# Optimization experiments

Measured on AMD Instinct MI355X. Metric: run time of the kernel, lower is better.

The kernel has to match this reference:

```python
import jax, jax.numpy as jnp
import numpy as np

NUM_HEADS = 8
FREQ_RATIO = 0.5


def _resize_bilinear(img, out_h, out_w):
    """Bilinear resize of last two dims, matching torch interpolate align_corners=False."""
    in_h, in_w = img.shape[-2], img.shape[-1]

    def idx(in_size, out_size):
        src = jnp.maximum((jnp.arange(out_size, dtype=jnp.float32) + 0.5) * (in_size / out_size) - 0.5, 0.0)
        i0 = jnp.floor(src).astype(jnp.int32)
        i1 = jnp.minimum(i0 + 1, in_size - 1)
        w = src - i0.astype(jnp.float32)
        return i0, i1, w

    r0, r1, wr = idx(in_h, out_h)
    img = img[..., r0, :] * (1.0 - wr)[:, None] + img[..., r1, :] * wr[:, None]
    c0, c1, wc = idx(in_w, out_w)
    img = img[..., c0] * (1.0 - wc) + img[..., c1] * wc
    return img


def setup_inputs() -> dict:
    key = jax.random.key(0)
    ks = jax.random.split(key, 6)
    B, T, J, C = 4, 256, 17, 512
    H = NUM_HEADS
    x = jax.random.normal(ks[0], (B, T, J, C), dtype=jnp.float32)
    att_map = jax.random.uniform(ks[1], (B, H, J, T, T), dtype=jnp.float32)
    weight = jax.random.uniform(ks[2], (1,), dtype=jnp.float32)
    w_qkv = jax.random.normal(ks[3], (C, 3 * C), dtype=jnp.float32) * 0.02
    w_proj = jax.random.normal(ks[4], (C, C), dtype=jnp.float32) * 0.02
    b_proj = jnp.zeros((C,), dtype=jnp.float32)
    freq_gate = jnp.ones((1,), dtype=jnp.float32)
    return {"x": x, "att_map": att_map, "weight": weight, "w_qkv": w_qkv,
            "w_proj": w_proj, "b_proj": b_proj, "freq_gate": freq_gate}


def reference(x, att_map, weight, w_qkv, w_proj, b_proj, freq_gate):
    B, T, J, C = x.shape
    H = NUM_HEADS
    d = C // H
    scale = d ** (-0.5)

    qkv = (x @ w_qkv).reshape(B, T, J, 3, H, d)
    qkv = jnp.transpose(qkv, (3, 0, 4, 2, 1, 5))  # [3,B,H,J,T,d]
    q, k, v = qkv[0], qkv[1], qkv[2]

    # time-domain attention over T, per (B,H,J)
    attn_time = jax.nn.softmax(jnp.einsum('bhjtd,bhjsd->bhjts', q, k) * scale, axis=-1)

    # frequency-domain attention
    qf = jnp.fft.rfft(q, axis=3)
    kf = jnp.fft.rfft(k, axis=3)
    F = qf.shape[3]                      # T//2 + 1
    keep = max(1, int(F * FREQ_RATIO))
    qf = qf[:, :, :, :keep]
    kf = kf[:, :, :, :keep]
    af = jnp.einsum('bhjfd,bhjgd->bhjfg', qf, jnp.conj(kf)) * scale  # complex [B,H,J,keep,keep]
    # torch combines softmax(real) + 1j*softmax(imag); only the real part survives
    af_real = jax.nn.softmax(af.real, axis=-1)
    af_real = jnp.pad(af_real, ((0, 0), (0, 0), (0, 0), (0, F - keep), (0, 0)))  # zero-pad rows to F
    attn_freq = _resize_bilinear(af_real, T, T)  # [B,H,J,T,T]

    gate = jax.nn.sigmoid(freq_gate)  # broadcastable scalar
    attn_self = gate * attn_freq + (1.0 - gate) * attn_time
    attn = weight * attn_self + (1.0 - weight) * att_map

    out = jnp.einsum('bhjts,bhjsd->bhjtd', attn, v)        # [B,H,J,T,d]
    out = jnp.transpose(out, (0, 3, 2, 1, 4)).reshape(B, T, J, C)
    return out @ w_proj + b_proj
```

## Files before the change

### kernel.cpp

```cpp
#include <hip/hip_runtime.h>
#include <hip/hip_bf16.h>


#define SCALE 0.125f
#define LSTR 72

typedef __attribute__((ext_vector_type(4))) float f32x4;
typedef __attribute__((ext_vector_type(8))) short bf16x8;
typedef __attribute__((ext_vector_type(8))) unsigned short u16x8;

__device__ __forceinline__ float bf2f(unsigned short u) {
  return __uint_as_float(((unsigned int)u) << 16);
}
__device__ __forceinline__ unsigned short f2bf(float f) {
  unsigned int u = __float_as_uint(f);
  u += 0x7FFFu + ((u >> 16) & 1u);
  return (unsigned short)(u >> 16);
}

__global__ __launch_bounds__(256) void conv_x(
    const float* __restrict__ x, unsigned short* __restrict__ xh,
    unsigned short* __restrict__ xl) {
  const size_t i = ((size_t)blockIdx.x * 256 + threadIdx.x) * 8;
  float4 a = *(const float4*)(x + i);
  float4 b = *(const float4*)(x + i + 4);
  float vv[8] = {a.x, a.y, a.z, a.w, b.x, b.y, b.z, b.w};
  u16x8 hi, lo;
#pragma unroll
  for (int e = 0; e < 8; ++e) {
    unsigned short h = f2bf(vv[e]);
    hi[e] = h;
    lo[e] = f2bf(vv[e] - bf2f(h));
  }
  *(u16x8*)&xh[i] = hi;
  *(u16x8*)&xl[i] = lo;
}

__global__ __launch_bounds__(256) void conv_wT(
    const float* __restrict__ w, unsigned short* __restrict__ th,
    unsigned short* __restrict__ tl, int N) {
  __shared__ float T[64][65];
  const int tid = threadIdx.x;
  const int nt = blockIdx.x * 64, kt = blockIdx.y * 64;
  for (int i = tid; i < 4096; i += 256) {
    const int r = i >> 6, c = i & 63;
    T[r][c] = w[(size_t)(kt + r) * N + nt + c];
  }
  __syncthreads();
  for (int i = tid; i < 4096; i += 256) {
    const int rn = i >> 6, ck = i & 63;
    const float v = T[ck][rn];
    const unsigned short h = f2bf(v);
    const size_t o = (size_t)(nt + rn) * 512 + kt + ck;
    th[o] = h;
    tl[o] = f2bf(v - bf2f(h));
  }
}

__global__ __launch_bounds__(256, 2) void qkv_gemm(
    const unsigned short* __restrict__ xh, const unsigned short* __restrict__ xl,
    const unsigned short* __restrict__ wh, const unsigned short* __restrict__ wl,
    unsigned short* __restrict__ qh, unsigned short* __restrict__ ql,
    unsigned short* __restrict__ kh, unsigned short* __restrict__ kl,
    unsigned short* __restrict__ vt) {
  __shared__ __attribute__((aligned(16))) unsigned short Wt[2][128 * LSTR];
  __shared__ __attribute__((aligned(16))) unsigned short Xt[2][128 * LSTR];

  const int tid = threadIdx.x;
  const int bx = blockIdx.x, by = blockIdx.y;
  const int wid = tid >> 6, lane = tid & 63;
  const int lr = lane & 15, lg = lane >> 4;
  const int wr = wid >> 1, wc = wid & 1;
  const int srow = tid >> 3, skg = tid & 7;

  const unsigned short* xhp = xh + (size_t)(by * 128 + srow) * 512 + skg * 8;
  const unsigned short* xlp = xl + (size_t)(by * 128 + srow) * 512 + skg * 8;
  const unsigned short* whp = wh + (size_t)(bx * 128 + srow) * 512 + skg * 8;
  const unsigned short* wlp = wl + (size_t)(bx * 128 + srow) * 512 + skg * 8;

  u16x8 rxh[4], rxl[4], rwh[4], rwl[4];
  auto loadk = [&](int k0) {
#pragma unroll
    for (int it = 0; it < 4; ++it) {
      const size_t o = (size_t)(32 * it) * 512 + k0;
      rxh[it] = *(const u16x8*)(xhp + o);
      rxl[it] = *(const u16x8*)(xlp + o);
      rwh[it] = *(const u16x8*)(whp + o);
      rwl[it] = *(const u16x8*)(wlp + o);
    }
  };

  f32x4 acc[4][4];
#pragma unroll
  for (int nt = 0; nt < 4; ++nt)
#pragma unroll
    for (int mt = 0; mt < 4; ++mt) acc[nt][mt] = (f32x4){0.f, 0.f, 0.f, 0.f};

  loadk(0);
  for (int s = 0; s < 8; ++s) {
    if (s) __syncthreads();
#pragma unroll
    for (int it = 0; it < 4; ++it) {
      const int base = (srow + 32 * it) * LSTR + skg * 8;
      *(u16x8*)&Xt[0][base] = rxh[it];
      *(u16x8*)&Xt[1][base] = rxl[it];
      *(u16x8*)&Wt[0][base] = rwh[it];
      *(u16x8*)&Wt[1][base] = rwl[it];
    }
    __syncthreads();
    if (s < 7) loadk((s + 1) * 64);
#pragma unroll
    for (int kh2 = 0; kh2 < 2; ++kh2) {
      const int kbase = kh2 * 32 + lg * 8;
      bf16x8 Ah[4], Al[4], Bh[4], Bl[4];
#pragma unroll
      for (int nt = 0; nt < 4; ++nt) {
        const int n = wr * 64 + nt * 16 + lr;
        Ah[nt] = *(bf16x8*)&Wt[0][n * LSTR + kbase];
        Al[nt] = *(bf16x8*)&Wt[1][n * LSTR + kbase];
      }
#pragma unroll
      for (int mt = 0; mt < 4; ++mt) {
        const int m = wc * 64 + mt * 16 + lr;
        Bh[mt] = *(bf16x8*)&Xt[0][m * LSTR + kbase];
        Bl[mt] = *(bf16x8*)&Xt[1][m * LSTR + kbase];
      }
#pragma unroll
      for (int nt = 0; nt < 4; ++nt)
#pragma unroll
        for (int mt = 0; mt < 4; ++mt) {
          acc[nt][mt] = __builtin_amdgcn_mfma_f32_16x16x32_bf16(Ah[nt], Bh[mt], acc[nt][mt], 0, 0, 0);
          acc[nt][mt] = __builtin_amdgcn_mfma_f32_16x16x32_bf16(Ah[nt], Bl[mt], acc[nt][mt], 0, 0, 0);
          acc[nt][mt] = __builtin_amdgcn_mfma_f32_16x16x32_bf16(Al[nt], Bh[mt], acc[nt][mt], 0, 0, 0);
        }
    }
  }

#pragma unroll
  for (int mt = 0; mt < 4; ++mt) {
    const int m = by * 128 + wc * 64 + mt * 16 + lr;
    const int jj = m % 17;
    const int bt = m / 17;
    const int t = bt & 255;
    const int b = bt >> 8;
#pragma unroll
    for (int nt = 0; nt < 4; ++nt) {
      const int c = bx * 128 + wr * 64 + nt * 16 + lg * 4;
      const int qi = c >> 9;
      const int h = (c >> 6) & 7;
      const int dd = c & 63;
      const size_t hdbase = ((size_t)((b * 8 + h) * 17 + jj)) * 16384;
      float a0 = acc[nt][mt][0], a1 = acc[nt][mt][1], a2 = acc[nt][mt][2],
            a3 = acc[nt][mt][3];
      ushort4 hi4 = make_ushort4(f2bf(a0), f2bf(a1), f2bf(a2), f2bf(a3));
      if (qi == 2) {
        vt[hdbase + (size_t)(dd + 0) * 256 + t] = hi4.x;
        vt[hdbase + (size_t)(dd + 1) * 256 + t] = hi4.y;
        vt[hdbase + (size_t)(dd + 2) * 256 + t] = hi4.z;
        vt[hdbase + (size_t)(dd + 3) * 256 + t] = hi4.w;
      } else {
        ushort4 lo4 = make_ushort4(f2bf(a0 - bf2f(hi4.x)), f2bf(a1 - bf2f(hi4.y)),
                                   f2bf(a2 - bf2f(hi4.z)), f2bf(a3 - bf2f(hi4.w)));
        unsigned short* dh = qi ? kh : qh;
        unsigned short* dl = qi ? kl : ql;
        *(ushort4*)&dh[hdbase + t * 64 + dd] = hi4;
        *(ushort4*)&dl[hdbase + t * 64 + dd] = lo4;
      }
    }
  }
}

__global__ __launch_bounds__(256) void freq_kernel(
    const unsigned short* __restrict__ qhp, const unsigned short* __restrict__ qlp,
    const unsigned short* __restrict__ khp, const unsigned short* __restrict__ klp,
    unsigned short* __restrict__ af_out) {
  __shared__ __attribute__((aligned(16))) unsigned short qT[2][64 * 256];
  __shared__ __attribute__((aligned(16))) unsigned short QF[4][64 * 64];
  __shared__ __attribute__((aligned(16))) unsigned short KF[4][64 * 64];

  const int tid = threadIdx.x;
  const int head = blockIdx.x;
  const int w = tid >> 6, lane = tid & 63;
  const int lr = lane & 15, lg = lane >> 4;
  const int f0 = w << 4;

  bf16x8 Ech[8], Ecl[8], Esh[8], Esl[8];
  {
    const int f = f0 + lr;
#pragma unroll
    for (int kb = 0; kb < 8; ++kb) {
      bf16x8 ch, cl, sh, sl;
#pragma unroll
      for (int i = 0; i < 8; ++i) {
        int t = kb * 32 + lg * 8 + i;
        int idx = (f * t) & 255;
        float s, c;
        __sincosf((float)idx * 0.02454369260617026f, &s, &c);
        unsigned short chh = f2bf(c);
        unsigned short shh = f2bf(s);
        ch[i] = (short)chh;
        cl[i] = (short)f2bf(c - bf2f(chh));
        sh[i] = (short)shh;
        sl[i] = (short)f2bf(s - bf2f(shh));
      }
      Ech[kb] = ch; Ecl[kb] = cl; Esh[kb] = sh; Esl[kb] = sl;
    }
  }

  for (int pass = 0; pass < 2; ++pass) {
    const unsigned short* sh_ = (pass ? khp : qhp) + head * 16384;
    const unsigned short* sl_ = (pass ? klp : qlp) + head * 16384;
    __syncthreads();
    for (int i = tid; i < 4096; i += 256) {
      int t = i >> 4, dq = i & 15;
      ushort4 hv = *(const ushort4*)&sh_[t * 64 + dq * 4];
      ushort4 lv = *(const ushort4*)&sl_[t * 64 + dq * 4];
      unsigned short hvv[4] = {hv.x, hv.y, hv.z, hv.w};
      unsigned short lvv[4] = {lv.x, lv.y, lv.z, lv.w};
#pragma unroll
      for (int c = 0; c < 4; ++c) {
        int d = dq * 4 + c;
        int byo = d * 512 + ((t * 2) ^ ((d & 31) << 4));
        *(unsigned short*)((char*)qT[0] + byo) = hvv[c];
        *(unsigned short*)((char*)qT[1] + byo) = lvv[c];
      }
    }
    __syncthreads();

    f32x4 ar[4], ai[4];
#pragma unroll
    for (int nt = 0; nt < 4; ++nt) {
      ar[nt] = (f32x4){0.f, 0.f, 0.f, 0.f};
      ai[nt] = (f32x4){0.f, 0.f, 0.f, 0.f};
    }
#pragma unroll
    for (int kb = 0; kb < 8; ++kb) {
#pragma unroll
      for (int nt = 0; nt < 4; ++nt) {
        const int d = nt * 16 + lr;
        const int byo = d * 512 + ((kb * 64 + lg * 16) ^ ((d & 31) << 4));
        bf16x8 bh = *(bf16x8*)((char*)qT[0] + byo);
        bf16x8 bl = *(bf16x8*)((char*)qT[1] + byo);
        ar[nt] = __builtin_amdgcn_mfma_f32_16x16x32_bf16(Ech[kb], bh, ar[nt], 0, 0, 0);
        ar[nt] = __builtin_amdgcn_mfma_f32_16x16x32_bf16(Ech[kb], bl, ar[nt], 0, 0, 0);
        ar[nt] = __builtin_amdgcn_mfma_f32_16x16x32_bf16(Ecl[kb], bh, ar[nt], 0, 0, 0);
        ai[nt] = __builtin_amdgcn_mfma_f32_16x16x32_bf16(Esh[kb], bh, ai[nt], 0, 0, 0);
        ai[nt] = __builtin_amdgcn_mfma_f32_16x16x32_bf16(Esh[kb], bl, ai[nt], 0, 0, 0);
        ai[nt] = __builtin_amdgcn_mfma_f32_16x16x32_bf16(Esl[kb], bh, ai[nt], 0, 0, 0);
      }
    }
    unsigned short(*DST)[64 * 64] = pass ? KF : QF;
#pragma unroll
    for (int nt = 0; nt < 4; ++nt) {
#pragma unroll
      for (int j = 0; j < 4; ++j) {
        const int f = f0 + lg * 4 + j;
        const int d = nt * 16 + lr;
        const int byo = f * 128 + ((d * 2) ^ ((f & 7) << 4));
        float vr = ar[nt][j], vi = ai[nt][j];
        unsigned short rh = f2bf(vr);
        unsigned short ih = f2bf(vi);
        *(unsigned short*)((char*)DST[0] + byo) = rh;
        *(unsigned short*)((char*)DST[1] + byo) = f2bf(vr - bf2f(rh));
        *(unsigned short*)((char*)DST[2] + byo) = ih;
        *(unsigned short*)((char*)DST[3] + byo) = f2bf(vi - bf2f(ih));
      }
    }
  }
  __syncthreads();

  f32x4 acc[4];
#pragma unroll
  for (int nt = 0; nt < 4; ++nt) acc[nt] = (f32x4){0.f, 0.f, 0.f, 0.f};
#pragma unroll
  for (int kb = 0; kb < 2; ++kb) {
    const int fA = f0 + lr;
    const int abyo = fA * 128 + ((kb * 64 + lg * 16) ^ ((fA & 7) << 4));
    bf16x8 arh = *(bf16x8*)((char*)QF[0] + abyo);
    bf16x8 arl = *(bf16x8*)((char*)QF[1] + abyo);
    bf16x8 aih = *(bf16x8*)((char*)QF[2] + abyo);
    bf16x8 ail = *(bf16x8*)((char*)QF[3] + abyo);
#pragma unroll
    for (int nt = 0; nt < 4; ++nt) {
      const int g = nt * 16 + lr;
      const int bbyo = g * 128 + ((kb * 64 + lg * 16) ^ ((g & 7) << 4));
      bf16x8 brh = *(bf16x8*)((char*)KF[0] + bbyo);
      bf16x8 brl = *(bf16x8*)((char*)KF[1] + bbyo);
      bf16x8 bih = *(bf16x8*)((char*)KF[2] + bbyo);
      bf16x8 bil = *(bf16x8*)((char*)KF[3] + bbyo);
      acc[nt] = __builtin_amdgcn_mfma_f32_16x16x32_bf16(arh, brh, acc[nt], 0, 0, 0);
      acc[nt] = __builtin_amdgcn_mfma_f32_16x16x32_bf16(arh, brl, acc[nt], 0, 0, 0);
      acc[nt] = __builtin_amdgcn_mfma_f32_16x16x32_bf16(arl, brh, acc[nt], 0, 0, 0);
      acc[nt] = __builtin_amdgcn_mfma_f32_16x16x32_bf16(aih, bih, acc[nt], 0, 0, 0);
      acc[nt] = __builtin_amdgcn_mfma_f32_16x16x32_bf16(aih, bil, acc[nt], 0, 0, 0);
      acc[nt] = __builtin_amdgcn_mfma_f32_16x16x32_bf16(ail, bih, acc[nt], 0, 0, 0);
    }
  }

  unsigned short* outh = af_out + head * 4096;
#pragma unroll
  for (int j = 0; j < 4; ++j) {
    float m = fmaxf(fmaxf(acc[0][j], acc[1][j]), fmaxf(acc[2][j], acc[3][j]));
#pragma unroll
    for (int mask = 1; mask < 16; mask <<= 1) m = fmaxf(m, __shfl_xor(m, mask));
    float e[4];
    float rs = 0.f;
#pragma unroll
    for (int nt = 0; nt < 4; ++nt) {
      e[nt] = __expf((acc[nt][j] - m) * SCALE);
      rs += e[nt];
    }
#pragma unroll
    for (int mask = 1; mask < 16; mask <<= 1) rs += __shfl_xor(rs, mask);
    const float inv = 1.0f / rs;
    const int f = f0 + lg * 4 + j;
#pragma unroll
    for (int nt = 0; nt < 4; ++nt) outh[f * 64 + nt * 16 + lr] = f2bf(e[nt] * inv);
  }
}

__global__ __launch_bounds__(256) void attn_kernel(
    const unsigned short* __restrict__ qhp, const unsigned short* __restrict__ khp,
    const unsigned short* __restrict__ vtp, const unsigned short* __restrict__ af,
    const float* __restrict__ att_map, const float* __restrict__ weight,
    const float* __restrict__ fgate, float* __restrict__ out_perm) {
  __shared__ unsigned short Ks[256 * 64];
  __shared__ unsigned short Vt[64 * 256];
  __shared__ unsigned short AFW[64 * 66];
  __shared__ unsigned short Psc[4][16 * 40];

  const int tid = threadIdx.x;
  const int head = blockIdx.x;
  const int jj = head % 17;
  const int hb = head / 17;
  const int h = hb & 7;
  const int b = hb >> 3;
  const int w = tid >> 6, lane = tid & 63;
  const int lr = lane & 15, lg = lane >> 4;

  const float* amh = att_map + (size_t)head * 65536;
  const unsigned short* qbase = qhp + head * 16384;

  const unsigned short* ksrc = khp + head * 16384;
  const unsigned short* vsrc = vtp + head * 16384;
  for (int i = tid; i < 2048; i += 256) {
    int s = i >> 3, dq8 = i & 7;
    u16x8 kv = *(const u16x8*)&ksrc[s * 64 + dq8 * 8];
    int koff = s * 128 + ((dq8 * 16) ^ ((s & 7) << 4));
    *(u16x8*)((char*)Ks + koff) = kv;
    int d = i >> 5, t8 = i & 31;
    u16x8 vv = *(const u16x8*)&vsrc[d * 256 + t8 * 8];
    int voff = d * 512 + ((t8 * 16) ^ ((d & 7) << 4));
    *(u16x8*)((char*)Vt + voff) = vv;
  }
  const unsigned short* asrc = af + head * 4096;
  for (int i = tid; i < 1024; i += 256) {
    int f = i >> 4, gq = (i & 15) << 2;
    *(ushort4*)&AFW[f * 66 + gq] = *(const ushort4*)&asrc[f * 64 + gq];
  }
  __syncthreads();

  const float wv = weight[0];
  const float gate = 1.0f / (1.0f + __expf(-fgate[0]));
  const float cg = wv * gate;
  const float cp = wv * (1.0f - gate);
  const float c2 = 1.0f - wv;
  unsigned short* psc = Psc[w];

  {
    const int fA = w * 16 + lr;
    f32x4 wacc[4];
#pragma unroll
    for (int nt = 0; nt < 4; ++nt) wacc[nt] = (f32x4){0.f, 0.f, 0.f, 0.f};
#pragma unroll
    for (int kc = 0; kc < 8; ++kc) {
      bf16x8 afr;
#pragma unroll
      for (int i = 0; i < 8; ++i) {
        const int s = kc * 32 + lg * 8 + i;
        float srcg = fmaxf((s + 0.5f) * 0.25f - 0.5f, 0.0f);
        int g0 = (int)srcg;
        float wc = srcg - (float)g0;
        int g1 = g0 + 1;
        if (g1 > 63) g1 = 63;
        float v = bf2f(AFW[fA * 66 + g0]) * (1.0f - wc) + bf2f(AFW[fA * 66 + g1]) * wc;
        afr[i] = (short)f2bf(v);
      }
      const int s0 = kc * 32 + lg * 8;
#pragma unroll
      for (int nt = 0; nt < 4; ++nt) {
        const int d = nt * 16 + lr;
        const int off = d * 512 + ((s0 * 2) ^ ((d & 7) << 4));
        bf16x8 bv = *(bf16x8*)((char*)Vt + off);
        wacc[nt] = __builtin_amdgcn_mfma_f32_16x16x32_bf16(afr, bv, wacc[nt], 0, 0, 0);
      }
    }
    __syncthreads();
#pragma unroll
    for (int nt = 0; nt < 4; ++nt) {
#pragma unroll
      for (int j = 0; j < 4; ++j) {
        AFW[(w * 16 + lg * 4 + j) * 66 + nt * 16 + lr] = f2bf(wacc[nt][j]);
      }
    }
    __syncthreads();
  }

  bf16x8 rq[2];
  {
    const unsigned short* qrow = qbase + (w * 64 + lr) * 64 + lg * 8;
    rq[0] = *(const bf16x8*)(qrow);
    rq[1] = *(const bf16x8*)(qrow + 32);
  }

  for (int tt = 0; tt < 4; ++tt) {
    const int tw = w * 64 + tt * 16;
    const float* amrow = amh + (size_t)(tw + lr) * 256 + lg * 8;

    bf16x8 aq[2] = {rq[0], rq[1]};

    f32x4 S[16];
#pragma unroll
    for (int nt = 0; nt < 16; ++nt) {
      f32x4 accv = {0.f, 0.f, 0.f, 0.f};
#pragma unroll
      for (int kc = 0; kc < 2; ++kc) {
        int srow = nt * 16 + lr;
        int d0 = kc * 32 + lg * 8;
        int off = srow * 128 + ((d0 * 2) ^ ((srow & 7) << 4));
        bf16x8 bk = *(bf16x8*)((char*)Ks + off);
        accv = __builtin_amdgcn_mfma_f32_16x16x32_bf16(aq[kc], bk, accv, 0, 0, 0);
      }
      S[nt] = accv;
    }

    if (tt < 3) {
      const unsigned short* qrow = qbase + (tw + 16 + lr) * 64 + lg * 8;
      rq[0] = *(const bf16x8*)(qrow);
      rq[1] = *(const bf16x8*)(qrow + 32);
    }

    float c1j[4];
#pragma unroll
    for (int j = 0; j < 4; ++j) {
      float m = -1e30f;
#pragma unroll
      for (int nt = 0; nt < 16; ++nt) m = fmaxf(m, S[nt][j]);
#pragma unroll
      for (int mask = 1; mask < 16; mask <<= 1) m = fmaxf(m, __shfl_xor(m, mask));
      float rs = 0.f;
#pragma unroll
      for (int nt = 0; nt < 16; ++nt) {
        float e = __expf((S[nt][j] - m) * SCALE);
        S[nt][j] = e;
        rs += e;
      }
#pragma unroll
      for (int mask = 1; mask < 16; mask <<= 1) rs += __shfl_xor(rs, mask);
      c1j[j] = cp / rs;
    }

    f32x4 O[4];
#pragma unroll
    for (int dt = 0; dt < 4; ++dt) O[dt] = (f32x4){0.f, 0.f, 0.f, 0.f};
    float4 am0 = *(const float4*)(amrow);
    float4 am1 = *(const float4*)(amrow + 4);
#pragma unroll
    for (int sb = 0; sb < 8; ++sb) {
      float4 nx0, nx1;
      if (sb < 7) {
        nx0 = *(const float4*)(amrow + (sb + 1) * 32);
        nx1 = *(const float4*)(amrow + (sb + 1) * 32 + 4);
      }
#pragma unroll
      for (int half = 0; half < 2; ++half) {
        const int nt = sb * 2 + half;
#pragma unroll
        for (int j = 0; j < 4; ++j) {
          psc[(lg * 4 + j) * 40 + half * 16 + lr] = f2bf(c1j[j] * S[nt][j]);
        }
      }
      bf16x8 praw = *(bf16x8*)&psc[lr * 40 + lg * 8];
      bf16x8 pa;
      {
        float av[8] = {am0.x, am0.y, am0.z, am0.w, am1.x, am1.y, am1.z, am1.w};
#pragma unroll
        for (int i = 0; i < 8; ++i) {
          pa[i] = (short)f2bf(bf2f((unsigned short)praw[i]) + c2 * av[i]);
        }
      }
      const int s0 = sb * 32 + lg * 8;
#pragma unroll
      for (int dt = 0; dt < 4; ++dt) {
        const int d = dt * 16 + lr;
        int off = d * 512 + ((s0 * 2) ^ ((d & 7) << 4));
        bf16x8 bv = *(bf16x8*)((char*)Vt + off);
        O[dt] = __builtin_amdgcn_mfma_f32_16x16x32_bf16(pa, bv, O[dt], 0, 0, 0);
      }
      am0 = nx0;
      am1 = nx1;
    }

#pragma unroll
    for (int j = 0; j < 4; ++j) {
      const int t = tw + lg * 4 + j;
      float srcf = fmaxf((t + 0.5f) * (129.0f / 256.0f) - 0.5f, 0.0f);
      int f0r = (int)srcf;
      float wf = srcf - (float)f0r;
      int f1r = f0r + 1;
      const bool v0 = (f0r < 64), v1 = (f1r < 64);
      float* orow = out_perm + ((size_t)((b * 256 + t) * 17 + jj)) * 512 + h * 64;
#pragma unroll
      for (int dt = 0; dt < 4; ++dt) {
        const int d = dt * 16 + lr;
        float fv = 0.f;
        if (v0) fv += (1.0f - wf) * bf2f(AFW[f0r * 66 + d]);
        if (v1) fv += wf * bf2f(AFW[f1r * 66 + d]);
        orow[d] = O[dt][j] + cg * fv;
      }
    }
  }
}

__global__ __launch_bounds__(256, 2) void proj_gemm(
    const float* __restrict__ A,
    const unsigned short* __restrict__ wh, const unsigned short* __restrict__ wl,
    const float* __restrict__ bias, float* __restrict__ out) {
  __shared__ __attribute__((aligned(16))) unsigned short Wt[2][128 * LSTR];
  __shared__ __attribute__((aligned(16))) unsigned short Xt[2][128 * LSTR];

  const int tid = threadIdx.x;
  const int bx = blockIdx.x, by = blockIdx.y;
  const int wid = tid >> 6, lane = tid & 63;
  const int lr = lane & 15, lg = lane >> 4;
  const int wr = wid >> 1, wc = wid & 1;
  const int srow = tid >> 3, skg = tid & 7;

  const float* ap = A + (size_t)(by * 128 + srow) * 512 + skg * 8;
  const unsigned short* whp = wh + (size_t)(bx * 128 + srow) * 512 + skg * 8;
  const unsigned short* wlp = wl + (size_t)(bx * 128 + srow) * 512 + skg * 8;

  float4 rA[4][2];
  u16x8 rwh[4], rwl[4];
  auto loadk = [&](int k0) {
#pragma unroll
    for (int it = 0; it < 4; ++it) {
      const size_t o = (size_t)(32 * it) * 512 + k0;
      rA[it][0] = *(const float4*)(ap + o);
      rA[it][1] = *(const float4*)(ap + o + 4);
      rwh[it] = *(const u16x8*)(whp + o);
      rwl[it] = *(const u16x8*)(wlp + o);
    }
  };

  f32x4 acc[4][4];
#pragma unroll
  for (int nt = 0; nt < 4; ++nt)
#pragma unroll
    for (int mt = 0; mt < 4; ++mt) acc[nt][mt] = (f32x4){0.f, 0.f, 0.f, 0.f};

  loadk(0);
  for (int s = 0; s < 8; ++s) {
    if (s) __syncthreads();
#pragma unroll
    for (int it = 0; it < 4; ++it) {
      const int base = (srow + 32 * it) * LSTR + skg * 8;
      float vv[8] = {rA[it][0].x, rA[it][0].y, rA[it][0].z, rA[it][0].w,
                     rA[it][1].x, rA[it][1].y, rA[it][1].z, rA[it][1].w};
      u16x8 hi, lo;
#pragma unroll
      for (int e = 0; e < 8; ++e) {
        unsigned short h = f2bf(vv[e]);
        hi[e] = h;
        lo[e] = f2bf(vv[e] - bf2f(h));
      }
      *(u16x8*)&Xt[0][base] = hi;
      *(u16x8*)&Xt[1][base] = lo;
      *(u16x8*)&Wt[0][base] = rwh[it];
      *(u16x8*)&Wt[1][base] = rwl[it];
    }
    __syncthreads();
    if (s < 7) loadk((s + 1) * 64);
#pragma unroll
    for (int kh2 = 0; kh2 < 2; ++kh2) {
      const int kbase = kh2 * 32 + lg * 8;
      bf16x8 Ah[4], Al[4], Bh[4], Bl[4];
#pragma unroll
      for (int nt = 0; nt < 4; ++nt) {
        const int n = wr * 64 + nt * 16 + lr;
        Ah[nt] = *(bf16x8*)&Wt[0][n * LSTR + kbase];
        Al[nt] = *(bf16x8*)&Wt[1][n * LSTR + kbase];
      }
#pragma unroll
      for (int mt = 0; mt < 4; ++mt) {
        const int m = wc * 64 + mt * 16 + lr;
        Bh[mt] = *(bf16x8*)&Xt[0][m * LSTR + kbase];
        Bl[mt] = *(bf16x8*)&Xt[1][m * LSTR + kbase];
      }
#pragma unroll
      for (int nt = 0; nt < 4; ++nt)
#pragma unroll
        for (int mt = 0; mt < 4; ++mt) {
          acc[nt][mt] = __builtin_amdgcn_mfma_f32_16x16x32_bf16(Ah[nt], Bh[mt], acc[nt][mt], 0, 0, 0);
          acc[nt][mt] = __builtin_amdgcn_mfma_f32_16x16x32_bf16(Ah[nt], Bl[mt], acc[nt][mt], 0, 0, 0);
          acc[nt][mt] = __builtin_amdgcn_mfma_f32_16x16x32_bf16(Al[nt], Bh[mt], acc[nt][mt], 0, 0, 0);
        }
    }
  }

#pragma unroll
  for (int mt = 0; mt < 4; ++mt) {
    const int m = by * 128 + wc * 64 + mt * 16 + lr;
#pragma unroll
    for (int nt = 0; nt < 4; ++nt) {
      const int n = bx * 128 + wr * 64 + nt * 16 + lg * 4;
      float4 bi = *(const float4*)&bias[n];
      *(float4*)&out[(size_t)m * 512 + n] =
          make_float4(acc[nt][mt][0] + bi.x, acc[nt][mt][1] + bi.y,
                      acc[nt][mt][2] + bi.z, acc[nt][mt][3] + bi.w);
    }
  }
}

extern "C" void kernel_launch(void* const* d_in, const int* in_sizes, int n_in,
                              void* d_out, int out_size, void* d_ws, size_t ws_size,
                              hipStream_t stream) {
  (void)in_sizes; (void)n_in; (void)out_size; (void)ws_size;
  const float* x = (const float*)d_in[0];
  const float* att_map = (const float*)d_in[1];
  const float* weight = (const float*)d_in[2];
  const float* w_qkv = (const float*)d_in[3];
  const float* w_proj = (const float*)d_in[4];
  const float* b_proj = (const float*)d_in[5];
  const float* fgate = (const float*)d_in[6];
  float* out = (float*)d_out;

  char* ws = (char*)d_ws;
  const size_t PB = 17825792;
  unsigned short* qh = (unsigned short*)(ws);
  unsigned short* ql = (unsigned short*)(ws + PB);
  unsigned short* kh = (unsigned short*)(ws + 2 * PB);
  unsigned short* kl = (unsigned short*)(ws + 3 * PB);
  unsigned short* vt = (unsigned short*)(ws + 4 * PB);
  unsigned short* af = (unsigned short*)(ws + 5 * PB);
  char* base = ws + 5 * PB + 4456448;
  unsigned short* xh = (unsigned short*)(base);
  unsigned short* xl = (unsigned short*)(base + PB);
  float* out_perm = (float*)(base);
  unsigned short* wqh = (unsigned short*)(base + 35651584);
  unsigned short* wql = (unsigned short*)(base + 35651584 + 1572864);
  unsigned short* wph = (unsigned short*)(base + 35651584 + 2 * 1572864);
  unsigned short* wpl = (unsigned short*)(base + 35651584 + 2 * 1572864 + 524288);

  conv_x<<<4352, 256, 0, stream>>>(x, xh, xl);
  conv_wT<<<dim3(24, 8), 256, 0, stream>>>(w_qkv, wqh, wql, 1536);
  conv_wT<<<dim3(8, 8), 256, 0, stream>>>(w_proj, wph, wpl, 512);
  qkv_gemm<<<dim3(12, 136), 256, 0, stream>>>(xh, xl, wqh, wql, qh, ql, kh, kl, vt);
  freq_kernel<<<544, 256, 0, stream>>>(qh, ql, kh, kl, af);
  attn_kernel<<<544, 256, 0, stream>>>(qh, kh, vt, af, att_map, weight, fgate,
                                       out_perm);
  proj_gemm<<<dim3(4, 136), 256, 0, stream>>>(out_perm, wph, wpl, b_proj, out);
}
```

Before: 379.1 us.

## Remap QKV GEMM row tiles to per-(b,j) time slices with XCD block swizzle

The QKV GEMM grid becomes 1D with a block-index swizzle across the 8 XCDs. Each M tile now covers 128 consecutive time steps for a single (batch, joint) pair instead of 128 consecutive flattened rows. The intent is that the output scatter into the [B,H,J,T,d] Q/K/V^T layouts becomes contiguous in t, giving coalesced stores, and that the swizzle improves L2 locality of the shared weight and x tiles. The trade-off is that x loads become strided by 17 rows, which makes input reads less contiguous.

After: 351.4 us. -7.3%, faster.

```diff
diff --git a/kernel.cpp b/kernel.cpp
--- a/kernel.cpp
+++ b/kernel.cpp
@@ -67,14 +67,22 @@
   __shared__ __attribute__((aligned(16))) unsigned short Xt[2][128 * LSTR];
 
   const int tid = threadIdx.x;
-  const int bx = blockIdx.x, by = blockIdx.y;
+  const int lin = blockIdx.x;
+  const int swz = (lin & 7) * 204 + (lin >> 3);
+  const int by = swz / 12, bx = swz % 12;
+  const int pair = by >> 1;
+  const int t0 = (by & 1) << 7;
+  const int b = pair / 17;
+  const int jj = pair % 17;
+
   const int wid = tid >> 6, lane = tid & 63;
   const int lr = lane & 15, lg = lane >> 4;
   const int wr = wid >> 1, wc = wid & 1;
   const int srow = tid >> 3, skg = tid & 7;
 
-  const unsigned short* xhp = xh + (size_t)(by * 128 + srow) * 512 + skg * 8;
-  const unsigned short* xlp = xl + (size_t)(by * 128 + srow) * 512 + skg * 8;
+  const size_t xrow0 = ((size_t)((b * 256 + t0 + srow) * 17 + jj)) * 512 + skg * 8;
+  const unsigned short* xhp = xh + xrow0;
+  const unsigned short* xlp = xl + xrow0;
   const unsigned short* whp = wh + (size_t)(bx * 128 + srow) * 512 + skg * 8;
   const unsigned short* wlp = wl + (size_t)(bx * 128 + srow) * 512 + skg * 8;
 
@@ -82,11 +90,12 @@
   auto loadk = [&](int k0) {
 #pragma unroll
     for (int it = 0; it < 4; ++it) {
-      const size_t o = (size_t)(32 * it) * 512 + k0;
-      rxh[it] = *(const u16x8*)(xhp + o);
-      rxl[it] = *(const u16x8*)(xlp + o);
-      rwh[it] = *(const u16x8*)(whp + o);
-      rwl[it] = *(const u16x8*)(wlp + o);
+      const size_t ox = (size_t)(32 * it) * 8704 + k0;
+      const size_t ow = (size_t)(32 * it) * 512 + k0;
+      rxh[it] = *(const u16x8*)(xhp + ox);
+      rxl[it] = *(const u16x8*)(xlp + ox);
+      rwh[it] = *(const u16x8*)(whp + ow);
+      rwl[it] = *(const u16x8*)(wlp + ow);
     }
   };
 
@@ -138,11 +147,7 @@
 
 #pragma unroll
   for (int mt = 0; mt < 4; ++mt) {
-    const int m = by * 128 + wc * 64 + mt * 16 + lr;
-    const int jj = m % 17;
-    const int bt = m / 17;
-    const int t = bt & 255;
-    const int b = bt >> 8;
+    const int t = t0 + wc * 64 + mt * 16 + lr;
 #pragma unroll
     for (int nt = 0; nt < 4; ++nt) {
       const int c = bx * 128 + wr * 64 + nt * 16 + lg * 4;
@@ -655,7 +660,7 @@
   conv_x<<<4352, 256, 0, stream>>>(x, xh, xl);
   conv_wT<<<dim3(24, 8), 256, 0, stream>>>(w_qkv, wqh, wql, 1536);
   conv_wT<<<dim3(8, 8), 256, 0, stream>>>(w_proj, wph, wpl, 512);
-  qkv_gemm<<<dim3(12, 136), 256, 0, stream>>>(xh, xl, wqh, wql, qh, ql, kh, kl, vt);
+  qkv_gemm<<<1632, 256, 0, stream>>>(xh, xl, wqh, wql, qh, ql, kh, kl, vt);
   freq_kernel<<<544, 256, 0, stream>>>(qh, ql, kh, kl, af);
   attn_kernel<<<544, 256, 0, stream>>>(qh, kh, vt, af, att_map, weight, fgate,
                                        out_perm);
```
